# Performance work log

Measured on AMD Instinct MI355X. Metric: run time of the kernel, lower is better.

## Reference

```python
import jax, jax.numpy as jnp
import numpy as np

N_SPIKES = 16384
N_UNITS = 256
N_NEIGHB = 128
RANK = 5
NC = 64
NC_OBS = 12
N_CAND = 10  # n_candidates*(n_search+1)+n_explore = 3*3+1
D = RANK * NC_OBS
LOG2PI = 1.8378770664093453


def setup_inputs() -> dict:
    key = jax.random.key(0)
    ks = jax.random.split(key, 8)
    features = jax.random.normal(ks[0], (N_SPIKES, RANK, NC_OBS), dtype=jnp.float32)
    mu = jax.random.normal(ks[1], (N_UNITS, RANK, NC), dtype=jnp.float32)
    # PSD inverse marginal covariances per neighborhood: A A^T / D + I
    A = jax.random.normal(ks[2], (N_NEIGHB, D, D), dtype=jnp.float32)
    Coo_inv = jnp.einsum('nij,nkj->nik', A, A) / D + jnp.eye(D, dtype=jnp.float32)
    # logdet of Coo = -logdet(Coo_inv)
    sign, ld = jnp.linalg.slogdet(Coo_inv)
    Coo_logdet = (-ld).astype(jnp.float32)
    log_proportions = jax.nn.log_softmax(jax.random.normal(ks[3], (N_UNITS,), dtype=jnp.float32))
    noise_log_prop = jnp.float32(-3.0)
    cands = jax.random.randint(ks[4], (N_SPIKES, N_CAND), 0, N_UNITS)
    nid = jax.random.randint(ks[5], (N_SPIKES,), 0, N_NEIGHB)
    # distinct observed channels per neighborhood, sorted
    perm = jnp.argsort(jax.random.uniform(ks[6], (N_NEIGHB, NC)), axis=1)
    obs_ix = jnp.sort(perm[:, :NC_OBS], axis=1)
    return {
        'features': features, 'mu': mu, 'Coo_inv': Coo_inv,
        'Coo_logdet': Coo_logdet, 'log_proportions': log_proportions,
        'noise_log_prop': noise_log_prop, 'cands': cands, 'nid': nid,
        'obs_ix': obs_ix,
    }


def reference(features, mu, Coo_inv, Coo_logdet, log_proportions, noise_log_prop, cands, nid, obs_ix):
    N, R, nco = features.shape
    Nu = mu.shape[0]
    C = cands.shape[1]
    Dd = R * nco
    # --- gather per-spike / per-candidate tables (load_batch) ---
    obs = obs_ix[nid]                                   # (N, nco)
    mu_c = mu[cands]                                    # (N, C, R, NC)
    nu = jnp.take_along_axis(mu_c, obs[:, None, None, :], axis=3)  # (N, C, R, nco)
    Cinv = Coo_inv[nid]                                 # (N, D, D)
    base = Coo_logdet[nid] + Dd * LOG2PI                # (N,)
    # --- truncated Gaussian log-likelihoods (te_batch) ---
    xf = features.reshape(N, Dd)
    xc = xf[:, None, :] - nu.reshape(N, C, Dd)          # (N, C, D)
    y = jnp.einsum('nde,nce->ncd', Cinv, xc)
    mahal = jnp.einsum('ncd,ncd->nc', y, xc)
    ll = log_proportions[cands] - 0.5 * (base[:, None] + mahal)
    yn = jnp.einsum('nde,ne->nd', Cinv, xf)
    mahal_noise = jnp.einsum('nd,nd->n', yn, xf)
    ll_noise = noise_log_prop - 0.5 * (base + mahal_noise)
    logliks = jnp.concatenate([ll, ll_noise[:, None]], axis=1)  # (N, C+1)
    Q = jax.nn.softmax(logliks, axis=1)
    # --- scatter-add sufficient statistics per unit ---
    Qc = Q[:, :C]
    seg = cands.reshape(-1)
    counts = jax.ops.segment_sum(Qc.reshape(-1), seg, num_segments=Nu)
    xw = (Qc[:, :, None] * xf[:, None, :]).reshape(N * C, Dd)
    xsum = jax.ops.segment_sum(xw, seg, num_segments=Nu)
    return jnp.concatenate([counts[:, None], xsum], axis=1)  # (Nu, D+1)
```

## Files before the change

kernel.cpp:

```cpp
#include <hip/hip_runtime.h>

#define N_SPIKES 16384
#define N_UNITS  256
#define N_NEIGHB 128
#define RANK     5
#define NC       64
#define NC_OBS   12
#define N_CAND   10
#define DD       60
#define DD4      15
#define OUT_COLS 61
#define OUT_SIZE (N_UNITS * OUT_COLS)
#define NSB      8
#define SCAP     192
#define CNT_PAD  4
#define CAP      1024

__global__ __launch_bounds__(512) void precompute_kernel(
    const float* __restrict__ mu, const float* __restrict__ Coo_inv,
    const int* __restrict__ obs_ix, const float* __restrict__ log_prop,
    float* __restrict__ w_buf, float* __restrict__ b_buf,
    int* __restrict__ gcount)
{
    __shared__ float nu_lds[128 * 61];
    __shared__ float q2_lds[128 * 4];

    const int b   = blockIdx.x;
    const int h   = b >> 1;
    const int ub  = (b & 1) * 128;
    const int tid = threadIdx.x;

    if (tid < 32) gcount[b * 32 + tid] = 0;

    {
        const int ut  = tid >> 2;
        const int dqt = tid & 3;
        const float* __restrict__ mub = mu + (ub + ut) * (RANK * NC);
#pragma unroll
        for (int j = 0; j < DD4; ++j) {
            const int d = dqt * DD4 + j;
            const int r = d / NC_OBS;
            const int jj = d - r * NC_OBS;
            const int ch = obs_ix[h * NC_OBS + jj];
            nu_lds[ut * 61 + d] = mub[r * NC + ch];
        }
    }
    __syncthreads();

    const int lane  = tid & 63;
    const int wave  = tid >> 6;
    const int ug    = wave >> 2;
    const int dq    = __builtin_amdgcn_readfirstlane(wave & 3);
    const int u_loc = ug * 64 + lane;
    const int u     = ub + u_loc;
    const int p     = h * N_UNITS + u;

    const float* __restrict__ Crow_base = Coo_inv + h * DD * DD + dq * DD4;

    float wreg[DD4];
#pragma unroll
    for (int j = 0; j < DD4; ++j) wreg[j] = 0.f;

    for (int e = 0; e < DD; ++e) {
        const float nu_e = nu_lds[u_loc * 61 + e];
        const float* __restrict__ Crow = Crow_base + e * DD;
#pragma unroll
        for (int j = 0; j < DD4; ++j)
            wreg[j] = fmaf(Crow[j], nu_e, wreg[j]);
    }

    float q2 = 0.f;
#pragma unroll
    for (int j = 0; j < DD4; ++j) q2 += wreg[j] * nu_lds[u_loc * 61 + dq * DD4 + j];
    q2_lds[u_loc * 4 + dq] = q2;

    float* __restrict__ wp = w_buf + p * DD + dq * DD4;
#pragma unroll
    for (int j = 0; j < DD4; ++j) wp[j] = wreg[j];

    __syncthreads();
    if ((wave & 3) == 0) {
        const float q2s = q2_lds[u_loc * 4 + 0] + q2_lds[u_loc * 4 + 1]
                        + q2_lds[u_loc * 4 + 2] + q2_lds[u_loc * 4 + 3];
        b_buf[p] = log_prop[u] - 0.5f * q2s;
    }
}

__global__ __launch_bounds__(1024) void spike_bin_kernel(
    const float* __restrict__ features, const float* __restrict__ noise_lp,
    const int* __restrict__ cands, const int* __restrict__ nid,
    const float* __restrict__ w_buf, const float* __restrict__ b_buf,
    int* __restrict__ gcount, int2* __restrict__ bins)
{
    const int tid  = threadIdx.x;
    const int lane = tid & 63;
    const int wave = tid >> 6;
    const int c    = lane & 15;
    const int s    = lane >> 4;
    const int n    = blockIdx.x * 64 + wave * 4 + s;
    const int sb   = blockIdx.x & (NSB - 1);
    const bool act = (c < N_CAND);
    const int cc   = act ? c : (N_CAND - 1);

    const float4* __restrict__ f4 = (const float4*)features;
    const float4* __restrict__ w4 = (const float4*)w_buf;

    const int   h   = nid[n];
    const float nlp = noise_lp[0];
    const int   uc  = cands[n * N_CAND + cc];
    const int   p   = h * N_UNITS + uc;
    const float bb  = b_buf[p];

    float t = 0.f;
#pragma unroll
    for (int k = 0; k < DD4; ++k) {
        const float4 wv = w4[p * DD4 + k];
        const float4 xv = f4[n * DD4 + k];
        t += wv.x * xv.x + wv.y * xv.y + wv.z * xv.z + wv.w * xv.w;
    }
    float ll = act ? (bb + t) : -3.4e38f;

    float m = ll;
    m = fmaxf(m, __shfl_xor(m, 1, 16));
    m = fmaxf(m, __shfl_xor(m, 2, 16));
    m = fmaxf(m, __shfl_xor(m, 4, 16));
    m = fmaxf(m, __shfl_xor(m, 8, 16));
    m = fmaxf(m, nlp);
    const float e = act ? __expf(ll - m) : 0.f;
    float ssum = e;
    ssum += __shfl_xor(ssum, 1, 16);
    ssum += __shfl_xor(ssum, 2, 16);
    ssum += __shfl_xor(ssum, 4, 16);
    ssum += __shfl_xor(ssum, 8, 16);
    ssum += __expf(nlp - m);
    const float q = e / ssum;

    if (act && q > 0.f) {
        const int bi  = uc * NSB + sb;
        const int pos = atomicAdd(&gcount[bi * CNT_PAD], 1);
        if (pos < SCAP) bins[bi * SCAP + pos] = make_int2(n, __float_as_int(q));
    }
}

__global__ __launch_bounds__(512) void unit_accum_kernel(
    const float* __restrict__ features, const int* __restrict__ gcount,
    const int2* __restrict__ bins, float* __restrict__ out)
{
    __shared__ int2  rec[CAP];
    __shared__ float red[8][OUT_COLS];
    __shared__ int   cnts[NSB];
    __shared__ int   offs[NSB + 1];

    const int u    = blockIdx.x;
    const int tid  = threadIdx.x;
    const int lane = tid & 63;
    const int wave = tid >> 6;

    if (tid < NSB) {
        int c = gcount[(u * NSB + tid) * CNT_PAD];
        cnts[tid] = c < SCAP ? c : SCAP;
    }
    __syncthreads();
    if (tid == 0) {
        int o = 0;
#pragma unroll
        for (int sb = 0; sb < NSB; ++sb) { offs[sb] = o; o += cnts[sb]; }
        offs[NSB] = o;
    }
    __syncthreads();

    {
        const int base = offs[wave];
        const int cnt  = cnts[wave];
        const int2* __restrict__ src = bins + (u * NSB + wave) * SCAP;
        for (int i = lane; i < cnt; i += 64) rec[base + i] = src[i];
    }
    __syncthreads();

    const int total = offs[NSB];
    const int g = tid >> 4;
    const int l = lane & 15;

    const float4* __restrict__ f4 = (const float4*)features;
    float4 a = {0.f, 0.f, 0.f, 0.f};
    float sq = 0.f;

#pragma unroll 2
    for (int i = g; i < total; i += 32) {
        const int2 r = rec[i];
        const float q = __int_as_float(r.y);
        if (l < DD4) {
            const float4 xv = f4[r.x * DD4 + l];
            a.x = fmaf(q, xv.x, a.x);
            a.y = fmaf(q, xv.y, a.y);
            a.z = fmaf(q, xv.z, a.z);
            a.w = fmaf(q, xv.w, a.w);
        } else if (l == DD4) {
            sq += q;
        }
    }

    a.x += __shfl_xor(a.x, 16, 64);  a.x += __shfl_xor(a.x, 32, 64);
    a.y += __shfl_xor(a.y, 16, 64);  a.y += __shfl_xor(a.y, 32, 64);
    a.z += __shfl_xor(a.z, 16, 64);  a.z += __shfl_xor(a.z, 32, 64);
    a.w += __shfl_xor(a.w, 16, 64);  a.w += __shfl_xor(a.w, 32, 64);
    sq  += __shfl_xor(sq, 16, 64);   sq  += __shfl_xor(sq, 32, 64);

    if (lane < DD4) {
        red[wave][1 + 4*lane + 0] = a.x;
        red[wave][1 + 4*lane + 1] = a.y;
        red[wave][1 + 4*lane + 2] = a.z;
        red[wave][1 + 4*lane + 3] = a.w;
    } else if (lane == DD4) {
        red[wave][0] = sq;
    }
    __syncthreads();

    if (tid < OUT_COLS) {
        float ssum = 0.f;
#pragma unroll
        for (int w = 0; w < 8; ++w) ssum += red[w][tid];
        out[u * OUT_COLS + tid] = ssum;
    }
}

extern "C" void kernel_launch(void* const* d_in, const int* in_sizes, int n_in,
                              void* d_out, int out_size, void* d_ws, size_t ws_size,
                              hipStream_t stream) {
    const float* features    = (const float*)d_in[0];
    const float* mu          = (const float*)d_in[1];
    const float* Coo_inv     = (const float*)d_in[2];
    const float* log_prop    = (const float*)d_in[4];
    const float* noise_lp    = (const float*)d_in[5];
    const int*   cands       = (const int*)d_in[6];
    const int*   nid         = (const int*)d_in[7];
    const int*   obs_ix      = (const int*)d_in[8];
    float* out = (float*)d_out;

    char* ws = (char*)d_ws;
    float* w_buf  = (float*)ws;
    float* b_buf  = (float*)(ws + 7864320);
    int*   gcount = (int*)(ws + 7995392);
    int2*  bins   = (int2*)(ws + 8028160);

    precompute_kernel<<<256, 512, 0, stream>>>(mu, Coo_inv, obs_ix, log_prop,
                                               w_buf, b_buf, gcount);
    spike_bin_kernel<<<256, 1024, 0, stream>>>(features, noise_lp, cands, nid,
                                               w_buf, b_buf, gcount, bins);
    unit_accum_kernel<<<256, 512, 0, stream>>>(features, gcount, bins, out);
}
```

Baseline: 112.4 us.

## Fuse three kernels into one cooperative kernel with grid syncs

Merges the precompute, spike-binning and per-unit accumulation kernels into one cooperative launch of 256 blocks of 1024 threads, separated by grid-wide barriers. This removes two kernel launch boundaries and their drain and refill gaps. In exchange, the precompute phase leaves half of each block's waves idle, and the grid syncs add their own cost. If the cooperative launch fails, the code falls back to the original three launches.

Measured after the change: 394.1 us. 251% more time.

```diff
diff --git a/kernel.cpp b/kernel.cpp
--- a/kernel.cpp
+++ b/kernel.cpp
@@ -1,4 +1,7 @@
 #include <hip/hip_runtime.h>
+#include <hip/hip_cooperative_groups.h>
+
+namespace cg = cooperative_groups;
 
 #define N_SPIKES 16384
 #define N_UNITS  256
@@ -14,7 +17,214 @@
 #define NSB      8
 #define SCAP     192
 #define CNT_PAD  4
-#define CAP      1024
+#define CAP      (NSB * SCAP)
+
+struct SmemP  { float nu[128 * 61]; float q2[128 * 4]; };
+struct SmemS2 { int2 rec[CAP]; float red[16][OUT_COLS]; int cnts[NSB]; int offs[NSB + 1]; };
+
+__global__ __launch_bounds__(1024) void fused_kernel(
+    const float* __restrict__ features, const float* __restrict__ mu,
+    const float* __restrict__ Coo_inv, const int* __restrict__ obs_ix,
+    const float* __restrict__ log_prop, const float* __restrict__ noise_lp,
+    const int* __restrict__ cands, const int* __restrict__ nid,
+    float* __restrict__ w_buf, float* __restrict__ b_buf,
+    int* __restrict__ gcount, int2* __restrict__ bins,
+    float* __restrict__ out)
+{
+    __shared__ __align__(16) char smem_raw[sizeof(SmemP) > sizeof(SmemS2) ?
+                                           sizeof(SmemP) : sizeof(SmemS2)];
+    cg::grid_group grid = cg::this_grid();
+
+    const int b    = blockIdx.x;
+    const int tid  = threadIdx.x;
+    const int lane = tid & 63;
+    const int wave = tid >> 6;
+
+    {
+        SmemP* sm = reinterpret_cast<SmemP*>(smem_raw);
+        const int h  = b >> 1;
+        const int ub = (b & 1) * 128;
+
+        if (tid < 32) gcount[b * 32 + tid] = 0;
+
+        if (tid < 512) {
+            const int ut  = tid >> 2;
+            const int dqt = tid & 3;
+            const float* __restrict__ mub = mu + (ub + ut) * (RANK * NC);
+#pragma unroll
+            for (int j = 0; j < DD4; ++j) {
+                const int d  = dqt * DD4 + j;
+                const int r  = d / NC_OBS;
+                const int jj = d - r * NC_OBS;
+                const int ch = obs_ix[h * NC_OBS + jj];
+                sm->nu[ut * 61 + d] = mub[r * NC + ch];
+            }
+        }
+        __syncthreads();
+
+        const int ug    = wave >> 2;
+        const int dq    = __builtin_amdgcn_readfirstlane(wave & 3);
+        const int u_loc = ug * 64 + lane;
+        const int u     = ub + u_loc;
+        const int p     = h * N_UNITS + u;
+
+        if (wave < 8) {
+            const float* __restrict__ Crow_base = Coo_inv + h * DD * DD + dq * DD4;
+            float wreg[DD4];
+#pragma unroll
+            for (int j = 0; j < DD4; ++j) wreg[j] = 0.f;
+
+            for (int e = 0; e < DD; ++e) {
+                const float nu_e = sm->nu[u_loc * 61 + e];
+                const float* __restrict__ Crow = Crow_base + e * DD;
+#pragma unroll
+                for (int j = 0; j < DD4; ++j)
+                    wreg[j] = fmaf(Crow[j], nu_e, wreg[j]);
+            }
+
+            float q2 = 0.f;
+#pragma unroll
+            for (int j = 0; j < DD4; ++j)
+                q2 += wreg[j] * sm->nu[u_loc * 61 + dq * DD4 + j];
+            sm->q2[u_loc * 4 + dq] = q2;
+
+            float* __restrict__ wp = w_buf + p * DD + dq * DD4;
+#pragma unroll
+            for (int j = 0; j < DD4; ++j) wp[j] = wreg[j];
+        }
+        __syncthreads();
+        if (wave < 8 && (wave & 3) == 0) {
+            const float q2s = sm->q2[u_loc * 4 + 0] + sm->q2[u_loc * 4 + 1]
+                            + sm->q2[u_loc * 4 + 2] + sm->q2[u_loc * 4 + 3];
+            b_buf[p] = log_prop[u] - 0.5f * q2s;
+        }
+    }
+
+    __threadfence();
+    grid.sync();
+
+    {
+        const int c    = lane & 15;
+        const int s    = lane >> 4;
+        const int n    = b * 64 + wave * 4 + s;
+        const int sb   = b & (NSB - 1);
+        const bool act = (c < N_CAND);
+        const int cc   = act ? c : (N_CAND - 1);
+
+        const float4* __restrict__ f4 = (const float4*)features;
+        const float4* __restrict__ w4 = (const float4*)w_buf;
+
+        const int   h   = nid[n];
+        const float nlp = noise_lp[0];
+        const int   uc  = cands[n * N_CAND + cc];
+        const int   p   = h * N_UNITS + uc;
+        const float bb  = b_buf[p];
+
+        float t = 0.f;
+#pragma unroll
+        for (int k = 0; k < DD4; ++k) {
+            const float4 wv = w4[p * DD4 + k];
+            const float4 xv = f4[n * DD4 + k];
+            t += wv.x * xv.x + wv.y * xv.y + wv.z * xv.z + wv.w * xv.w;
+        }
+        float ll = act ? (bb + t) : -3.4e38f;
+
+        float m = ll;
+        m = fmaxf(m, __shfl_xor(m, 1, 16));
+        m = fmaxf(m, __shfl_xor(m, 2, 16));
+        m = fmaxf(m, __shfl_xor(m, 4, 16));
+        m = fmaxf(m, __shfl_xor(m, 8, 16));
+        m = fmaxf(m, nlp);
+        const float e = act ? __expf(ll - m) : 0.f;
+        float ssum = e;
+        ssum += __shfl_xor(ssum, 1, 16);
+        ssum += __shfl_xor(ssum, 2, 16);
+        ssum += __shfl_xor(ssum, 4, 16);
+        ssum += __shfl_xor(ssum, 8, 16);
+        ssum += __expf(nlp - m);
+        const float q = e / ssum;
+
+        if (act && q > 0.f) {
+            const int bi  = uc * NSB + sb;
+            const int pos = atomicAdd(&gcount[bi * CNT_PAD], 1);
+            if (pos < SCAP) bins[bi * SCAP + pos] = make_int2(n, __float_as_int(q));
+        }
+    }
+
+    __threadfence();
+    grid.sync();
+
+    {
+        SmemS2* sm = reinterpret_cast<SmemS2*>(smem_raw);
+        const int u = b;
+
+        if (tid < NSB) {
+            int c = gcount[(u * NSB + tid) * CNT_PAD];
+            sm->cnts[tid] = c < SCAP ? c : SCAP;
+        }
+        __syncthreads();
+        if (tid == 0) {
+            int o = 0;
+#pragma unroll
+            for (int sb = 0; sb < NSB; ++sb) { sm->offs[sb] = o; o += sm->cnts[sb]; }
+            sm->offs[NSB] = o;
+        }
+        __syncthreads();
+
+        if (wave < NSB) {
+            const int base = sm->offs[wave];
+            const int cnt  = sm->cnts[wave];
+            const int2* __restrict__ src = bins + (u * NSB + wave) * SCAP;
+            for (int i = lane; i < cnt; i += 64) sm->rec[base + i] = src[i];
+        }
+        __syncthreads();
+
+        const int total = sm->offs[NSB];
+        const int g = tid >> 4;
+        const int l = lane & 15;
+
+        const float4* __restrict__ f4 = (const float4*)features;
+        float4 a = {0.f, 0.f, 0.f, 0.f};
+        float sq = 0.f;
+
+        for (int i = g; i < total; i += 64) {
+            const int2 r = sm->rec[i];
+            const float q = __int_as_float(r.y);
+            if (l < DD4) {
+                const float4 xv = f4[r.x * DD4 + l];
+                a.x = fmaf(q, xv.x, a.x);
+                a.y = fmaf(q, xv.y, a.y);
+                a.z = fmaf(q, xv.z, a.z);
+                a.w = fmaf(q, xv.w, a.w);
+            } else if (l == DD4) {
+                sq += q;
+            }
+        }
+
+        a.x += __shfl_xor(a.x, 16, 64);  a.x += __shfl_xor(a.x, 32, 64);
+        a.y += __shfl_xor(a.y, 16, 64);  a.y += __shfl_xor(a.y, 32, 64);
+        a.z += __shfl_xor(a.z, 16, 64);  a.z += __shfl_xor(a.z, 32, 64);
+        a.w += __shfl_xor(a.w, 16, 64);  a.w += __shfl_xor(a.w, 32, 64);
+        sq  += __shfl_xor(sq, 16, 64);   sq  += __shfl_xor(sq, 32, 64);
+
+        if (lane < DD4) {
+            sm->red[wave][1 + 4*lane + 0] = a.x;
+            sm->red[wave][1 + 4*lane + 1] = a.y;
+            sm->red[wave][1 + 4*lane + 2] = a.z;
+            sm->red[wave][1 + 4*lane + 3] = a.w;
+        } else if (lane == DD4) {
+            sm->red[wave][0] = sq;
+        }
+        __syncthreads();
+
+        if (tid < OUT_COLS) {
+            float ssum = 0.f;
+#pragma unroll
+            for (int w = 0; w < 16; ++w) ssum += sm->red[w][tid];
+            out[u * OUT_COLS + tid] = ssum;
+        }
+    }
+}
 
 __global__ __launch_bounds__(512) void precompute_kernel(
     const float* __restrict__ mu, const float* __restrict__ Coo_inv,
@@ -185,7 +395,6 @@
     float4 a = {0.f, 0.f, 0.f, 0.f};
     float sq = 0.f;
 
-#pragma unroll 2
     for (int i = g; i < total; i += 32) {
         const int2 r = rec[i];
         const float q = __int_as_float(r.y);
@@ -243,9 +452,19 @@
     int*   gcount = (int*)(ws + 7995392);
     int2*  bins   = (int2*)(ws + 8028160);
 
-    precompute_kernel<<<256, 512, 0, stream>>>(mu, Coo_inv, obs_ix, log_prop,
-                                               w_buf, b_buf, gcount);
-    spike_bin_kernel<<<256, 1024, 0, stream>>>(features, noise_lp, cands, nid,
-                                               w_buf, b_buf, gcount, bins);
-    unit_accum_kernel<<<256, 512, 0, stream>>>(features, gcount, bins, out);
+    void* args[] = {
+        (void*)&features, (void*)&mu, (void*)&Coo_inv, (void*)&obs_ix,
+        (void*)&log_prop, (void*)&noise_lp, (void*)&cands, (void*)&nid,
+        (void*)&w_buf, (void*)&b_buf, (void*)&gcount, (void*)&bins, (void*)&out
+    };
+    hipError_t err = hipLaunchCooperativeKernel(
+        (const void*)fused_kernel, dim3(256), dim3(1024), args, 0, stream);
+
+    if (err != hipSuccess) {
+        precompute_kernel<<<256, 512, 0, stream>>>(mu, Coo_inv, obs_ix, log_prop,
+                                                   w_buf, b_buf, gcount);
+        spike_bin_kernel<<<256, 1024, 0, stream>>>(features, noise_lp, cands, nid,
+                                                   w_buf, b_buf, gcount, bins);
+        unit_accum_kernel<<<256, 512, 0, stream>>>(features, gcount, bins, out);
+    }
 }
```
